# Kernel optimization log

Measured on AMD Instinct MI355X. Metric: run time of the kernel, lower is better.

The kernel has to match this reference:

```python
import jax, jax.numpy as jnp
import numpy as np

B, N, NODE_DIM, EDGE_DIM, H, L, Z, OUT = 4, 512, 16, 8, 64, 3, 64, 1
EPS = 1e-5  # torch BatchNorm1d default eps, training-mode batch stats


def _bn(x, g, b):
    # BatchNorm1d in training mode: biased batch mean/var over batch axis
    m = jnp.mean(x, axis=0)
    v = jnp.var(x, axis=0)
    return g * (x - m) * jax.lax.rsqrt(v + EPS) + b


def setup_inputs():
    keys = jax.random.split(jax.random.key(0), 16)

    def g(k, shape):
        fan = (shape[-2] + shape[-1]) if len(shape) >= 2 else 2 * shape[-1]
        return (jax.random.normal(k, shape) * np.sqrt(2.0 / fan)).astype(jnp.float32)

    return {
        'adj': (jax.random.uniform(keys[0], (B, N, N)) < 0.1).astype(jnp.float32),
        'node_feat': jax.random.normal(keys[1], (B, N, NODE_DIM), dtype=jnp.float32),
        'edge_feat': jax.random.normal(keys[2], (B, N, N, EDGE_DIM), dtype=jnp.float32),
        'nf1_w': g(keys[3], (NODE_DIM, 256)), 'nf1_b': jnp.zeros((256,), jnp.float32),
        'nf2_w': g(keys[4], (256, H)), 'nf2_b': jnp.zeros((H,), jnp.float32),
        'ef1_w': g(keys[5], (EDGE_DIM, 256)), 'ef1_b': jnp.zeros((256,), jnp.float32),
        'ef2_w': g(keys[6], (256, H)), 'ef2_b': jnp.zeros((H,), jnp.float32),
        'gcn_w': g(keys[7], (L, H, H)),
        'vn1_w': g(keys[8], (L, H, 2 * H)), 'vn1_b': jnp.zeros((L, 2 * H), jnp.float32),
        'vn1_g': jnp.ones((L, 2 * H), jnp.float32), 'vn1_be': jnp.zeros((L, 2 * H), jnp.float32),
        'vn2_w': g(keys[9], (L, 2 * H, H)), 'vn2_b': jnp.zeros((L, H), jnp.float32),
        'vn2_g': jnp.ones((L, H), jnp.float32), 'vn2_be': jnp.zeros((L, H), jnp.float32),
        'comb_w': g(keys[10], (L, 2 * H, H)), 'comb_b': jnp.zeros((L, H), jnp.float32),
        'lat1_w': g(keys[11], ((L + 1) * H, 256)), 'lat1_b': jnp.zeros((256,), jnp.float32),
        'lat2_w': g(keys[12], (256, Z)), 'lat2_b': jnp.zeros((Z,), jnp.float32),
        'fc1_w': g(keys[13], (Z, 512)), 'fc1_b': jnp.zeros((512,), jnp.float32),
        'fc2_w': g(keys[14], (512, OUT)), 'fc2_b': jnp.zeros((OUT,), jnp.float32),
    }


def _forward(adj, node_feat, edge_feat, nf1_w, nf1_b, nf2_w, nf2_b, ef1_w, ef1_b,
             ef2_w, ef2_b, gcn_w, vn1_w, vn1_b, vn1_g, vn1_be, vn2_w, vn2_b, vn2_g,
             vn2_be, comb_w, comb_b, lat1_w, lat1_b, lat2_w, lat2_b, fc1_w, fc1_b,
             fc2_w, fc2_b):
    # node / edge embedding MLPs
    nh = jnp.tanh(node_feat @ nf1_w + nf1_b)
    nh = jnp.tanh(nh @ nf2_w + nf2_b)                       # [B,N,H]
    eh = jnp.tanh(edge_feat @ ef1_w + ef1_b)
    eh = jnp.tanh(eh @ ef2_w + ef2_b)                       # [B,N,N,H]
    # einsum 'bijc,bjk->bik' sums over both j and c -> reduce c first
    e_sum = jnp.sum(eh, axis=-1)                            # [B,N,N]
    # GCN normalization: D = 1/rowsum(adj + I); identical every layer
    dinv = 1.0 / (jnp.sum(adj, axis=-1) + 1.0)
    adj_n = dinv[:, :, None] * adj                          # [B,N,N]
    hidden = nh
    alls = [nh]
    for l in range(L):
        hidden = jnp.tanh(adj_n @ (hidden @ gcn_w[l]))      # GraphConvSparse
        vn = jnp.mean(hidden, axis=1)                       # virtual-node pool [B,H]
        vn = jax.nn.relu(_bn(vn @ vn1_w[l] + vn1_b[l], vn1_g[l], vn1_be[l]))
        vn = jax.nn.relu(_bn(vn @ vn2_w[l] + vn2_b[l], vn2_g[l], vn2_be[l]))
        hidden = hidden + vn[:, None, :]                    # broadcast back to nodes
        gated = jnp.tanh(jnp.einsum('bij,bjk->bik', e_sum, hidden))
        hidden = jnp.tanh(jnp.concatenate([hidden, gated], axis=-1) @ comb_w[l] + comb_b[l])
        alls.append(hidden)
    lat = jnp.tanh(jnp.concatenate(alls, axis=-1) @ lat1_w + lat1_b)
    lat = jnp.tanh(lat @ lat2_w + lat2_b)                   # [B,N,Z]
    lat_sum = jnp.sum(lat, axis=1)                          # [B,Z]
    h = jnp.tanh(lat_sum @ fc1_w + fc1_b)
    predict = h @ fc2_w + fc2_b                             # [B,OUT]
    return predict, lat_sum


def reference(adj, node_feat, edge_feat, nf1_w, nf1_b, nf2_w, nf2_b, ef1_w, ef1_b,
              ef2_w, ef2_b, gcn_w, vn1_w, vn1_b, vn1_g, vn1_be, vn2_w, vn2_b, vn2_g,
              vn2_be, comb_w, comb_b, lat1_w, lat1_b, lat2_w, lat2_b, fc1_w, fc1_b,
              fc2_w, fc2_b):
    return _forward(adj, node_feat, edge_feat, nf1_w, nf1_b, nf2_w, nf2_b, ef1_w,
                    ef1_b, ef2_w, ef2_b, gcn_w, vn1_w, vn1_b, vn1_g, vn1_be, vn2_w,
                    vn2_b, vn2_g, vn2_be, comb_w, comb_b, lat1_w, lat1_b, lat2_w,
                    lat2_b, fc1_w, fc1_b, fc2_w, fc2_b)
```

## Files before the change

### kernel.cpp

```cpp
#include <hip/hip_runtime.h>
#include <math.h>

typedef unsigned short u16;
typedef unsigned int u32;

typedef __attribute__((ext_vector_type(8))) short short8;
typedef __attribute__((ext_vector_type(4))) float floatx4;

#define NTILES 16384

__device__ __forceinline__ float bfu(u16 u) { return __uint_as_float(((u32)u) << 16); }
__device__ __forceinline__ u16 f2bfs(float f) {
  u32 x = __float_as_uint(f);
  return (u16)((x + 0x7FFFu + ((x >> 16) & 1u)) >> 16);
}
__device__ __forceinline__ float tanh_fast(float x) {
  float e = __builtin_amdgcn_exp2f(x * 2.885390081777927f);
  return 1.0f - 2.0f * __builtin_amdgcn_rcpf(e + 1.0f);
}

__global__ __attribute__((amdgpu_flat_work_group_size(1024, 1024)))
__attribute__((amdgpu_waves_per_eu(4, 4)))
void k_edge(const float* __restrict__ ef,
    const float* __restrict__ w1, const float* __restrict__ b1,
    const float* __restrict__ w2, const float* __restrict__ b2,
    float* __restrict__ es32, u16* __restrict__ es16, int use16) {
  __shared__ __align__(16) short T1[16 * 2048];
  __shared__ __align__(16) short W2L[16384];
  __shared__ __align__(16) short W1L[2 * 2056];
  __shared__ __align__(16) float B1L[256];
  __shared__ __align__(16) float B2L[64];
  int t = threadIdx.x;
  int lane = t & 63, w = t >> 6, q = lane >> 4, r = lane & 15;

  for (int u = 0; u < 16; ++u) {
    int flat = u * 1024 + t;
    int k = flat >> 6, n = flat & 63;
    int c = k >> 3, j = k & 7;
    int physc = (c & 16) | ((c & 15) ^ (n & 15));
    W2L[(n * 32 + physc) * 8 + j] = (short)f2bfs(w2[flat]);
  }
  if (t < 512) {
    int hilo = t >> 8, idx = t & 255;
    int gu = idx >> 4, rr = idx & 15;
    int feat = (gu < 8) ? (rr * 8 + gu) : (120 + rr * 8 + gu);
    short8 v;
#pragma unroll
    for (int j = 0; j < 8; ++j) {
      float x = w1[j * 256 + feat];
      u32 xb = __float_as_uint(x);
      u16 hi = (u16)(xb >> 16);
      v[j] = hilo ? (short)f2bfs(x - bfu(hi)) : (short)hi;
    }
    *(short8*)&W1L[hilo * 2056 + idx * 8] = v;
  }
  if (t < 256) B1L[t] = b1[t];
  if (t < 64)  B2L[t] = b2[t];
  __syncthreads();

  short* t1w = &T1[w * 2048];
  const int hb = (q >> 1) * 2056;
  const int nw = gridDim.x * 16;
  int qt = blockIdx.x * 16 + w;
  float4 e0, e1;
  {
    const float4* ep = (const float4*)(ef + (size_t)qt * 128 + (size_t)r * 8);
    e0 = ep[0]; e1 = ep[1];
  }

  for (; qt < 4 * NTILES; qt += nw) {
    float ev[8] = {e0.x, e0.y, e0.z, e0.w, e1.x, e1.y, e1.z, e1.w};
    short8 af1;
#pragma unroll
    for (int j = 0; j < 8; ++j) {
      u32 xb = __float_as_uint(ev[j]);
      u16 hi = (u16)(xb >> 16);
      af1[j] = (q & 1) ? (short)f2bfs(ev[j] - bfu(hi)) : (short)hi;
    }
    int nqt = qt + nw;
    if (nqt < 4 * NTILES) {
      const float4* ep = (const float4*)(ef + (size_t)nqt * 128 + (size_t)r * 8);
      e0 = ep[0]; e1 = ep[1];
    }
    floatx4 acc4[4];
#pragma unroll
    for (int nt = 0; nt < 4; ++nt) acc4[nt] = (floatx4){0.f, 0.f, 0.f, 0.f};
#pragma unroll
    for (int ph = 0; ph < 2; ++ph) {
      floatx4 c1[8];
#pragma unroll
      for (int u = 0; u < 8; ++u) c1[u] = (floatx4){0.f, 0.f, 0.f, 0.f};
#pragma unroll
      for (int u = 0; u < 8; ++u) {
        short8 bf = *(const short8*)&W1L[hb + ((ph * 8 + u) * 16 + r) * 8];
        c1[u] = __builtin_amdgcn_mfma_f32_16x16x32_bf16(af1, bf, c1[u], 0, 0, 0);
      }
      asm volatile("s_waitcnt lgkmcnt(0)" ::: "memory");
      __builtin_amdgcn_sched_barrier(0);
      const float4* bp = (const float4*)&B1L[ph * 128 + r * 8];
      float4 bA = bp[0], bB = bp[1];
      float bias[8] = {bA.x, bA.y, bA.z, bA.w, bB.x, bB.y, bB.z, bB.w};
#pragma unroll
      for (int reg = 0; reg < 4; ++reg) {
        u32 pk[4];
#pragma unroll
        for (int p2 = 0; p2 < 4; ++p2) {
          float va = tanh_fast(c1[2 * p2][reg] + bias[2 * p2]);
          float vb = tanh_fast(c1[2 * p2 + 1][reg] + bias[2 * p2 + 1]);
          u32 pr;
          asm("v_cvt_pk_bf16_f32 %0, %1, %2" : "=v"(pr) : "v"(va), "v"(vb));
          pk[p2] = pr;
        }
        int row = q * 4 + reg;
        int physc = r ^ row;
        int4 wa; wa.x = (int)pk[0]; wa.y = (int)pk[1]; wa.z = (int)pk[2]; wa.w = (int)pk[3];
        *(int4*)&t1w[(row * 16 + physc) * 8] = wa;
      }
      asm volatile("s_waitcnt lgkmcnt(0)" ::: "memory");
      __builtin_amdgcn_sched_barrier(0);
#pragma unroll
      for (int sm = 0; sm < 4; ++sm) {
        int cc = (4 * sm + q) ^ r;
        short8 af = *(const short8*)&t1w[(r * 16 + cc) * 8];
        int wc = ph * 16 + cc;
#pragma unroll
        for (int nt = 0; nt < 4; ++nt) {
          short8 bf = *(const short8*)&W2L[((nt * 16 + r) * 32 + wc) * 8];
          acc4[nt] = __builtin_amdgcn_mfma_f32_16x16x32_bf16(af, bf, acc4[nt], 0, 0, 0);
        }
      }
    }
    float s0 = 0.f, s1 = 0.f, s2 = 0.f, s3 = 0.f;
#pragma unroll
    for (int nt = 0; nt < 4; ++nt) {
      float bb = B2L[nt * 16 + r];
      s0 += tanh_fast(acc4[nt][0] + bb);
      s1 += tanh_fast(acc4[nt][1] + bb);
      s2 += tanh_fast(acc4[nt][2] + bb);
      s3 += tanh_fast(acc4[nt][3] + bb);
    }
#pragma unroll
    for (int off = 1; off < 16; off <<= 1) {
      s0 += __shfl_xor(s0, off, 64);
      s1 += __shfl_xor(s1, off, 64);
      s2 += __shfl_xor(s2, off, 64);
      s3 += __shfl_xor(s3, off, 64);
    }
    if (r == 0) {
      int base = qt * 16 + q * 4;
      if (use16) {
        es16[base] = f2bfs(s0); es16[base + 1] = f2bfs(s1);
        es16[base + 2] = f2bfs(s2); es16[base + 3] = f2bfs(s3);
      } else {
        float4 o; o.x = s0; o.y = s1; o.z = s2; o.w = s3;
        *(float4*)&es32[base] = o;
      }
    }
  }
}

__global__ __launch_bounds__(256) void k_pre(const float* __restrict__ nf,
    const float* __restrict__ w1, const float* __restrict__ b1,
    const float* __restrict__ w2, const float* __restrict__ b2,
    const float* __restrict__ gw, const float* __restrict__ adj,
    float* __restrict__ hid, u16* __restrict__ alls16, float* __restrict__ tmp,
    float* __restrict__ dinv, int* __restrict__ cnt) {
  __shared__ float nfx[4][16];
  __shared__ float t1[4][256];
  __shared__ float nh[4][64];
  int t = threadIdx.x;
  int node0 = blockIdx.x * 4;
  if (blockIdx.x == 0 && t < 16) cnt[t] = 0;
  if (t < 64) nfx[t >> 4][t & 15] = nf[node0 * 16 + t];
  __syncthreads();
  float b1t = b1[t];
  float a0 = b1t, a1 = b1t, a2 = b1t, a3 = b1t;
#pragma unroll
  for (int c = 0; c < 16; ++c) {
    float wv = w1[c * 256 + t];
    a0 += nfx[0][c] * wv; a1 += nfx[1][c] * wv;
    a2 += nfx[2][c] * wv; a3 += nfx[3][c] * wv;
  }
  t1[0][t] = tanh_fast(a0); t1[1][t] = tanh_fast(a1);
  t1[2][t] = tanh_fast(a2); t1[3][t] = tanh_fast(a3);
  __syncthreads();
  int nl = t >> 6, h = t & 63;
  {
    float acc = b2[h];
    for (int c = 0; c < 256; c += 4) {
      float4 xv = *(const float4*)&t1[nl][c];
      acc += xv.x * w2[c * 64 + h] + xv.y * w2[(c + 1) * 64 + h]
           + xv.z * w2[(c + 2) * 64 + h] + xv.w * w2[(c + 3) * 64 + h];
    }
    float v = tanh_fast(acc);
    int node = node0 + nl;
    hid[node * 64 + h] = v;
    alls16[node * 256 + h] = f2bfs(v);
    nh[nl][h] = v;
  }
  __syncthreads();
  {
    float g = 0.f;
    for (int c = 0; c < 64; ++c) g += nh[nl][c] * gw[c * 64 + h];
    tmp[(node0 + nl) * 64 + h] = g;
  }
  {
    int lane = t & 63, row = node0 + (t >> 6);
    float s = 0.f;
#pragma unroll
    for (int u = 0; u < 8; ++u) s += adj[(size_t)row * 512 + u * 64 + lane];
#pragma unroll
    for (int off = 32; off > 0; off >>= 1) s += __shfl_xor(s, off, 64);
    if (lane == 0) dinv[row] = 1.0f / (s + 1.0f);
  }
}

__global__ __launch_bounds__(256) void k_adjmm0(const float* __restrict__ adj,
    const float* __restrict__ X, const float* __restrict__ dinv,
    float* __restrict__ out, float* __restrict__ vnpart, int* cnt,
    const float* __restrict__ vw1, const float* __restrict__ vb1,
    const float* __restrict__ vg1, const float* __restrict__ vbe1,
    const float* __restrict__ vw2, const float* __restrict__ vb2,
    const float* __restrict__ vg2, const float* __restrict__ vbe2,
    float* __restrict__ vnout, int l) {
  __shared__ float Xt[64 * 64];
  __shared__ float Al[8 * 65];
  __shared__ floatx4 red4[256];
  __shared__ int isLast;
  int t = threadIdx.x;
  int b = blockIdx.x >> 6, it = blockIdx.x & 63;
  int hq = t & 15, slot = t >> 4, row = slot & 7, half = slot >> 3;
  floatx4 acc = (floatx4){0.f, 0.f, 0.f, 0.f};
  for (int jt = 0; jt < 8; ++jt) {
    __syncthreads();
    for (int u = 0; u < 16; ++u) {
      int idx = u * 256 + t;
      int jl = idx >> 6, hh = idx & 63;
      Xt[idx] = X[(b * 512 + jt * 64 + jl) * 64 + hh];
    }
#pragma unroll
    for (int u = 0; u < 2; ++u) {
      int idx = u * 256 + t;
      int il = idx >> 6, jl = idx & 63;
      Al[il * 65 + jl] = adj[((size_t)(b * 512 + it * 8 + il)) * 512 + jt * 64 + jl];
    }
    __syncthreads();
    const float* xp = &Xt[(half * 32) * 64 + hq * 4];
    const float* ap = &Al[row * 65 + half * 32];
#pragma unroll
    for (int jl = 0; jl < 32; ++jl) {
      floatx4 xv = *(const floatx4*)(xp + jl * 64);
      float a = ap[jl];
      acc[0] += a * xv[0]; acc[1] += a * xv[1];
      acc[2] += a * xv[2]; acc[3] += a * xv[3];
    }
  }
  red4[t] = acc;
  __syncthreads();
  if (t < 128) {
    floatx4 s = red4[t], s2 = red4[t + 128];
    int gr = b * 512 + it * 8 + row;
    float d = dinv[gr];
    floatx4 o;
#pragma unroll
    for (int i = 0; i < 4; ++i) o[i] = tanh_fast((s[i] + s2[i]) * d);
    *(floatx4*)&out[gr * 64 + hq * 4] = o;
    red4[t] = o;
  }
  __syncthreads();
  if (t < 16) {
    floatx4 ssum = (floatx4){0.f, 0.f, 0.f, 0.f};
#pragma unroll
    for (int r2 = 0; r2 < 8; ++r2) {
      floatx4 v = red4[r2 * 16 + t];
      ssum[0] += v[0]; ssum[1] += v[1]; ssum[2] += v[2]; ssum[3] += v[3];
    }
    *(floatx4*)&vnpart[(b * 64 + it) * 64 + t * 4] = ssum;
  }
  __threadfence();
  __syncthreads();
  if (t == 0) isLast = (atomicAdd(cnt, 1) == 255);
  __syncthreads();
  if (isLast) {
    __threadfence();
    float* x0 = Xt; float* x1 = Xt + 256; float* y1 = Xt + 768; float* x2 = Xt + 1280;
    {
      int bb = t >> 6, h = t & 63;
      float s = 0.f;
      for (int c = 0; c < 64; ++c) s += vnpart[(bb * 64 + c) * 64 + h];
      x0[t] = s * (1.0f / 512.0f);
    }
    __syncthreads();
    for (int rep = 0; rep < 2; ++rep) {
      int idx = rep * 256 + t;
      int bb = idx >> 7, j = idx & 127;
      float a = vb1[l * 128 + j];
      for (int h = 0; h < 64; ++h) a += x0[bb * 64 + h] * vw1[l * 8192 + h * 128 + j];
      x1[idx] = a;
    }
    __syncthreads();
    if (t < 128) {
      int j = t;
      float a = x1[j], bq = x1[128 + j], c = x1[256 + j], d = x1[384 + j];
      float m = 0.25f * (a + bq + c + d);
      float da = a - m, db = bq - m, dc = c - m, dd = d - m;
      float var = 0.25f * (da * da + db * db + dc * dc + dd * dd);
      float sc = vg1[l * 128 + j] / sqrtf(var + 1e-5f);
      float be = vbe1[l * 128 + j];
      y1[j]       = fmaxf(sc * da + be, 0.f);
      y1[128 + j] = fmaxf(sc * db + be, 0.f);
      y1[256 + j] = fmaxf(sc * dc + be, 0.f);
      y1[384 + j] = fmaxf(sc * dd + be, 0.f);
    }
    __syncthreads();
    {
      int bb = t >> 6, k = t & 63;
      float a = vb2[l * 64 + k];
      for (int j = 0; j < 128; ++j) a += y1[bb * 128 + j] * vw2[l * 8192 + j * 64 + k];
      x2[t] = a;
    }
    __syncthreads();
    if (t < 64) {
      int k = t;
      float a = x2[k], bq = x2[64 + k], c = x2[128 + k], d = x2[192 + k];
      float m = 0.25f * (a + bq + c + d);
      float da = a - m, db = bq - m, dc = c - m, dd = d - m;
      float var = 0.25f * (da * da + db * db + dc * dc + dd * dd);
      float sc = vg2[l * 64 + k] / sqrtf(var + 1e-5f);
      float be = vbe2[l * 64 + k];
      vnout[k]       = fmaxf(sc * da + be, 0.f);
      vnout[64 + k]  = fmaxf(sc * db + be, 0.f);
      vnout[128 + k] = fmaxf(sc * dc + be, 0.f);
      vnout[192 + k] = fmaxf(sc * dd + be, 0.f);
    }
  }
}

__global__ __launch_bounds__(256) void k_gate_comb(
    const float* __restrict__ es32, const u16* __restrict__ es16, int use16,
    const float* __restrict__ hid, const float* __restrict__ vnin,
    const float* __restrict__ cw, const float* __restrict__ cb,
    const float* __restrict__ gw_next,
    u16* __restrict__ alls16, float* __restrict__ tmpout, int l, int do_gcn) {
  __shared__ float Xt[64 * 64];
  __shared__ float Al[8 * 65];
  __shared__ floatx4 red4[256];
  __shared__ float gatedL[8 * 64];
  __shared__ float catL[8 * 128];
  __shared__ float hnL[8 * 64];
  int t = threadIdx.x;
  int b = blockIdx.x >> 6, it = blockIdx.x & 63;
  int hq = t & 15, slot = t >> 4, row = slot & 7, half = slot >> 3;
  floatx4 acc = (floatx4){0.f, 0.f, 0.f, 0.f};
  for (int jt = 0; jt < 8; ++jt) {
    __syncthreads();
    for (int u = 0; u < 16; ++u) {
      int idx = u * 256 + t;
      int jl = idx >> 6, hh = idx & 63;
      Xt[idx] = hid[(b * 512 + jt * 64 + jl) * 64 + hh] + vnin[b * 64 + hh];
    }
#pragma unroll
    for (int u = 0; u < 2; ++u) {
      int idx = u * 256 + t;
      int il = idx >> 6, jl = idx & 63;
      size_t ai = ((size_t)(b * 512 + it * 8 + il)) * 512 + jt * 64 + jl;
      Al[il * 65 + jl] = use16 ? bfu(es16[ai]) : es32[ai];
    }
    __syncthreads();
    const float* xp = &Xt[(half * 32) * 64 + hq * 4];
    const float* ap = &Al[row * 65 + half * 32];
#pragma unroll
    for (int jl = 0; jl < 32; ++jl) {
      floatx4 xv = *(const floatx4*)(xp + jl * 64);
      float a = ap[jl];
      acc[0] += a * xv[0]; acc[1] += a * xv[1];
      acc[2] += a * xv[2]; acc[3] += a * xv[3];
    }
  }
  red4[t] = acc;
  __syncthreads();
  if (t < 128) {
    floatx4 s = red4[t], s2 = red4[t + 128];
    floatx4 o;
#pragma unroll
    for (int i = 0; i < 4; ++i) o[i] = tanh_fast(s[i] + s2[i]);
    *(floatx4*)&gatedL[row * 64 + hq * 4] = o;
  }
  __syncthreads();
#pragma unroll
  for (int u = 0; u < 4; ++u) {
    int idx = u * 256 + t;
    int nl = idx >> 7, c = idx & 127;
    int node = b * 512 + it * 8 + nl;
    catL[idx] = (c < 64) ? (hid[node * 64 + c] + vnin[b * 64 + c])
                         : gatedL[nl * 64 + (c - 64)];
  }
  __syncthreads();
  int nl = t >> 6, h = t & 63;
  float a0 = cb[l * 64 + h], a1 = a0;
  const float* wp = cw + l * 8192 + h;
  for (int c = 0; c < 128; ++c) {
    float wv = wp[c * 64];
    a0 += catL[nl * 128 + c] * wv;
    a1 += catL[(nl + 4) * 128 + c] * wv;
  }
  float v0 = tanh_fast(a0), v1 = tanh_fast(a1);
  int n0 = b * 512 + it * 8 + nl, n1 = n0 + 4;
  alls16[n0 * 256 + (l + 1) * 64 + h] = f2bfs(v0);
  alls16[n1 * 256 + (l + 1) * 64 + h] = f2bfs(v1);
  if (do_gcn) {
    hnL[nl * 64 + h] = v0;
    hnL[(nl + 4) * 64 + h] = v1;
    __syncthreads();
    float g0 = 0.f, g1 = 0.f;
    for (int c = 0; c < 64; ++c) {
      float wv = gw_next[c * 64 + h];
      g0 += hnL[nl * 64 + c] * wv;
      g1 += hnL[(nl + 4) * 64 + c] * wv;
    }
    tmpout[n0 * 64 + h] = g0;
    tmpout[n1 * 64 + h] = g1;
  }
}

__global__ __launch_bounds__(512) void k_lat(const u16* __restrict__ alls16,
    const float* __restrict__ w1, const float* __restrict__ bb1,
    const float* __restrict__ w2, const float* __restrict__ bb2,
    float* __restrict__ latpart) {
  __shared__ float x[8][256];
  __shared__ float t1[8][256];
  __shared__ float red[8][256];
  int t = threadIdx.x;
  int g = t >> 8, tt = t & 255;
  int b = blockIdx.x >> 6, chunk = blockIdx.x & 63;
#pragma unroll
  for (int u = 0; u < 4; ++u)
    x[g * 4 + u][tt] = bfu(alls16[(size_t)(b * 512 + chunk * 8 + g * 4 + u) * 256 + tt]);
  __syncthreads();
  float a1[4];
  float bb = bb1[tt];
#pragma unroll
  for (int u = 0; u < 4; ++u) a1[u] = bb;
  for (int c = 0; c < 256; ++c) {
    float wv = w1[c * 256 + tt];
#pragma unroll
    for (int u = 0; u < 4; ++u) a1[u] += x[g * 4 + u][c] * wv;
  }
#pragma unroll
  for (int u = 0; u < 4; ++u) t1[g * 4 + u][tt] = tanh_fast(a1[u]);
  __syncthreads();
  int quar = tt >> 6, k = tt & 63, c0 = quar * 64;
  float a2[4];
#pragma unroll
  for (int u = 0; u < 4; ++u) a2[u] = 0.f;
  for (int c = 0; c < 64; ++c) {
    float wv = w2[(c0 + c) * 64 + k];
#pragma unroll
    for (int u = 0; u < 4; ++u) a2[u] += t1[g * 4 + u][c0 + c] * wv;
  }
#pragma unroll
  for (int u = 0; u < 4; ++u) red[g * 4 + u][tt] = a2[u];
  __syncthreads();
  if (t < 64) {
    float acc2 = 0.f;
    float b2v = bb2[t];
#pragma unroll
    for (int u = 0; u < 8; ++u) {
      float s = red[u][t] + red[u][t + 64] + red[u][t + 128] + red[u][t + 192] + b2v;
      acc2 += tanh_fast(s);
    }
    latpart[(b * 64 + chunk) * 64 + t] = acc2;
  }
}

__global__ __launch_bounds__(512) void k_final(const float* __restrict__ latpart,
    const float* __restrict__ f1w, const float* __restrict__ f1b,
    const float* __restrict__ f2w, const float* __restrict__ f2b,
    float* __restrict__ outp) {
  __shared__ float lred[512];
  __shared__ float ls[64];
  __shared__ float wred[8];
  int b = blockIdx.x, t = threadIdx.x;
  int z = t & 63, cg = t >> 6;
  float s = 0.f;
  for (int c = cg * 8; c < cg * 8 + 8; ++c) s += latpart[(b * 64 + c) * 64 + z];
  lred[t] = s;
  __syncthreads();
  if (t < 64) {
    float ssum = 0.f;
    for (int gg = 0; gg < 8; ++gg) ssum += lred[gg * 64 + t];
    ls[t] = ssum;
    outp[4 + b * 64 + t] = ssum;
  }
  __syncthreads();
  float acc = f1b[t];
  for (int zz = 0; zz < 64; ++zz) acc += ls[zz] * f1w[zz * 512 + t];
  float h = tanh_fast(acc);
  float p = h * f2w[t];
#pragma unroll
  for (int off = 32; off > 0; off >>= 1) p += __shfl_xor(p, off, 64);
  if ((t & 63) == 0) wred[t >> 6] = p;
  __syncthreads();
  if (t == 0) {
    float a = 0.f;
    for (int wv = 0; wv < 8; ++wv) a += wred[wv];
    outp[b] = a + f2b[0];
  }
}

extern "C" void kernel_launch(void* const* d_in, const int* in_sizes, int n_in,
                              void* d_out, int out_size, void* d_ws, size_t ws_size,
                              hipStream_t stream) {
  const float* adj       = (const float*)d_in[0];
  const float* node_feat = (const float*)d_in[1];
  const float* edge_feat = (const float*)d_in[2];
  const float* nf1_w = (const float*)d_in[3];
  const float* nf1_b = (const float*)d_in[4];
  const float* nf2_w = (const float*)d_in[5];
  const float* nf2_b = (const float*)d_in[6];
  const float* ef1_w = (const float*)d_in[7];
  const float* ef1_b = (const float*)d_in[8];
  const float* ef2_w = (const float*)d_in[9];
  const float* ef2_b = (const float*)d_in[10];
  const float* gcn_w = (const float*)d_in[11];
  const float* vn1_w = (const float*)d_in[12];
  const float* vn1_b = (const float*)d_in[13];
  const float* vn1_g = (const float*)d_in[14];
  const float* vn1_be = (const float*)d_in[15];
  const float* vn2_w = (const float*)d_in[16];
  const float* vn2_b = (const float*)d_in[17];
  const float* vn2_g = (const float*)d_in[18];
  const float* vn2_be = (const float*)d_in[19];
  const float* comb_w = (const float*)d_in[20];
  const float* comb_b = (const float*)d_in[21];
  const float* lat1_w = (const float*)d_in[22];
  const float* lat1_b = (const float*)d_in[23];
  const float* lat2_w = (const float*)d_in[24];
  const float* lat2_b = (const float*)d_in[25];
  const float* fc1_w = (const float*)d_in[26];
  const float* fc1_b = (const float*)d_in[27];
  const float* fc2_w = (const float*)d_in[28];
  const float* fc2_b = (const float*)d_in[29];

  const int use16 = (ws_size < (size_t)12 * 1024 * 1024) ? 1 : 0;
  char* p = (char*)d_ws;
  float* es32 = (float*)p;
  u16*   es16 = (u16*)p;
  size_t es_bytes = use16 ? (size_t)1048576 * 2 : (size_t)1048576 * 4;
  u16*   alls16  = (u16*)(p + es_bytes);
  float* hid     = (float*)(alls16 + 524288);
  float* tmp     = hid + 131072;
  float* dinv    = tmp + 131072;
  float* vnpart  = dinv + 2048;
  float* vn      = vnpart + 16384;
  float* latpart = vn + 256;
  int*   cnt     = (int*)(latpart + 16384);

  k_pre<<<512, 256, 0, stream>>>(node_feat, nf1_w, nf1_b, nf2_w, nf2_b,
                                 gcn_w, adj, hid, alls16, tmp, dinv, cnt);
  k_edge<<<256, 1024, 0, stream>>>(edge_feat, ef1_w, ef1_b, ef2_w, ef2_b,
                                   es32, es16, use16);
  for (int l = 0; l < 3; ++l) {
    k_adjmm0<<<256, 256, 0, stream>>>(adj, tmp, dinv, hid, vnpart, cnt + l,
        vn1_w, vn1_b, vn1_g, vn1_be, vn2_w, vn2_b, vn2_g, vn2_be, vn, l);
    k_gate_comb<<<256, 256, 0, stream>>>(es32, es16, use16, hid, vn,
        comb_w, comb_b, gcn_w + (l + 1) * 4096, alls16, tmp, l, (l < 2) ? 1 : 0);
  }
  k_lat<<<256, 512, 0, stream>>>(alls16, lat1_w, lat1_b, lat2_w, lat2_b, latpart);
  k_final<<<4, 512, 0, stream>>>(latpart, fc1_w, fc1_b, fc2_w, fc2_b,
                                 (float*)d_out);
}
```

Before: 435.6 us.

## Halve rows per block and register-prefetch next tiles in adjacency matmul kernels

k_adjmm0 and k_gate_comb now give each block 4 node rows instead of 8, which doubles the grid to 512 blocks, and the inter-block counter and vnpart layout are resized to match. Each thread loads the next 64-column X and adjacency tile into registers while the current tile is computed from shared memory, so global-load latency overlaps the FMA loop. The aim is more blocks to fill the CUs and fewer stalls on global memory. In exchange, each X tile is re-read by twice as many blocks, more registers are used, and the per-block split of the reduction shrinks.

```diff
diff --git a/kernel.cpp b/kernel.cpp
--- a/kernel.cpp
+++ b/kernel.cpp
@@ -224,31 +224,40 @@
     const float* __restrict__ vg2, const float* __restrict__ vbe2,
     float* __restrict__ vnout, int l) {
   __shared__ float Xt[64 * 64];
-  __shared__ float Al[8 * 65];
+  __shared__ float Al[4 * 65];
   __shared__ floatx4 red4[256];
+  __shared__ floatx4 vnp4[64];
   __shared__ int isLast;
   int t = threadIdx.x;
-  int b = blockIdx.x >> 6, it = blockIdx.x & 63;
-  int hq = t & 15, slot = t >> 4, row = slot & 7, half = slot >> 3;
+  int b = blockIdx.x >> 7, blk = blockIdx.x & 127;
+  int hq = t & 15, slot = t >> 4, row = slot & 3, half = slot >> 2;
   floatx4 acc = (floatx4){0.f, 0.f, 0.f, 0.f};
+  float xreg[16], areg;
+  int il = t >> 6, jl2 = t & 63;
+#pragma unroll
+  for (int u = 0; u < 16; ++u) {
+    int jl = (u * 256 + t) >> 6;
+    xreg[u] = X[(b * 512 + jl) * 64 + jl2];
+  }
+  areg = adj[((size_t)(b * 512 + blk * 4 + il)) * 512 + jl2];
   for (int jt = 0; jt < 8; ++jt) {
     __syncthreads();
-    for (int u = 0; u < 16; ++u) {
-      int idx = u * 256 + t;
-      int jl = idx >> 6, hh = idx & 63;
-      Xt[idx] = X[(b * 512 + jt * 64 + jl) * 64 + hh];
-    }
-#pragma unroll
-    for (int u = 0; u < 2; ++u) {
-      int idx = u * 256 + t;
-      int il = idx >> 6, jl = idx & 63;
-      Al[il * 65 + jl] = adj[((size_t)(b * 512 + it * 8 + il)) * 512 + jt * 64 + jl];
-    }
-    __syncthreads();
-    const float* xp = &Xt[(half * 32) * 64 + hq * 4];
-    const float* ap = &Al[row * 65 + half * 32];
-#pragma unroll
-    for (int jl = 0; jl < 32; ++jl) {
+#pragma unroll
+    for (int u = 0; u < 16; ++u) Xt[u * 256 + t] = xreg[u];
+    Al[il * 65 + jl2] = areg;
+    __syncthreads();
+    if (jt < 7) {
+#pragma unroll
+      for (int u = 0; u < 16; ++u) {
+        int jl = (u * 256 + t) >> 6;
+        xreg[u] = X[(b * 512 + (jt + 1) * 64 + jl) * 64 + jl2];
+      }
+      areg = adj[((size_t)(b * 512 + blk * 4 + il)) * 512 + (jt + 1) * 64 + jl2];
+    }
+    const float* xp = &Xt[(half * 16) * 64 + hq * 4];
+    const float* ap = &Al[row * 65 + half * 16];
+#pragma unroll
+    for (int jl = 0; jl < 16; ++jl) {
       floatx4 xv = *(const floatx4*)(xp + jl * 64);
       float a = ap[jl];
       acc[0] += a * xv[0]; acc[1] += a * xv[1];
@@ -257,29 +266,27 @@
   }
   red4[t] = acc;
   __syncthreads();
-  if (t < 128) {
-    floatx4 s = red4[t], s2 = red4[t + 128];
-    int gr = b * 512 + it * 8 + row;
+  if (t < 64) {
+    floatx4 s0 = red4[t], s1 = red4[t + 64], s2 = red4[t + 128], s3 = red4[t + 192];
+    int gr = b * 512 + blk * 4 + (t >> 4);
     float d = dinv[gr];
     floatx4 o;
 #pragma unroll
-    for (int i = 0; i < 4; ++i) o[i] = tanh_fast((s[i] + s2[i]) * d);
-    *(floatx4*)&out[gr * 64 + hq * 4] = o;
-    red4[t] = o;
+    for (int i = 0; i < 4; ++i) o[i] = tanh_fast((((s0[i] + s1[i]) + s2[i]) + s3[i]) * d);
+    *(floatx4*)&out[gr * 64 + (t & 15) * 4] = o;
+    vnp4[t] = o;
   }
   __syncthreads();
   if (t < 16) {
-    floatx4 ssum = (floatx4){0.f, 0.f, 0.f, 0.f};
-#pragma unroll
-    for (int r2 = 0; r2 < 8; ++r2) {
-      floatx4 v = red4[r2 * 16 + t];
-      ssum[0] += v[0]; ssum[1] += v[1]; ssum[2] += v[2]; ssum[3] += v[3];
-    }
-    *(floatx4*)&vnpart[(b * 64 + it) * 64 + t * 4] = ssum;
+    floatx4 s = vnp4[t], s1 = vnp4[16 + t], s2 = vnp4[32 + t], s3 = vnp4[48 + t];
+    floatx4 ss;
+#pragma unroll
+    for (int i = 0; i < 4; ++i) ss[i] = ((s[i] + s1[i]) + s2[i]) + s3[i];
+    *(floatx4*)&vnpart[(b * 128 + blk) * 64 + t * 4] = ss;
   }
   __threadfence();
   __syncthreads();
-  if (t == 0) isLast = (atomicAdd(cnt, 1) == 255);
+  if (t == 0) isLast = (atomicAdd(cnt, 1) == 511);
   __syncthreads();
   if (isLast) {
     __threadfence();
@@ -287,7 +294,7 @@
     {
       int bb = t >> 6, h = t & 63;
       float s = 0.f;
-      for (int c = 0; c < 64; ++c) s += vnpart[(bb * 64 + c) * 64 + h];
+      for (int c = 0; c < 128; ++c) s += vnpart[(bb * 128 + c) * 64 + h];
       x0[t] = s * (1.0f / 512.0f);
     }
     __syncthreads();
@@ -343,34 +350,46 @@
     const float* __restrict__ gw_next,
     u16* __restrict__ alls16, float* __restrict__ tmpout, int l, int do_gcn) {
   __shared__ float Xt[64 * 64];
-  __shared__ float Al[8 * 65];
+  __shared__ float Al[4 * 65];
   __shared__ floatx4 red4[256];
-  __shared__ float gatedL[8 * 64];
-  __shared__ float catL[8 * 128];
-  __shared__ float hnL[8 * 64];
+  __shared__ float gatedL[4 * 64];
+  __shared__ float catL[4 * 128];
+  __shared__ float hnL[4 * 64];
   int t = threadIdx.x;
-  int b = blockIdx.x >> 6, it = blockIdx.x & 63;
-  int hq = t & 15, slot = t >> 4, row = slot & 7, half = slot >> 3;
+  int b = blockIdx.x >> 7, blk = blockIdx.x & 127;
+  int hq = t & 15, slot = t >> 4, row = slot & 3, half = slot >> 2;
+  int il = t >> 6, jl2 = t & 63;
+  float vnl = vnin[b * 64 + jl2];
   floatx4 acc = (floatx4){0.f, 0.f, 0.f, 0.f};
+  float xreg[16], areg;
+#pragma unroll
+  for (int u = 0; u < 16; ++u) {
+    int jl = (u * 256 + t) >> 6;
+    xreg[u] = hid[(b * 512 + jl) * 64 + jl2];
+  }
+  {
+    size_t ai = ((size_t)(b * 512 + blk * 4 + il)) * 512 + jl2;
+    areg = use16 ? bfu(es16[ai]) : es32[ai];
+  }
   for (int jt = 0; jt < 8; ++jt) {
     __syncthreads();
-    for (int u = 0; u < 16; ++u) {
-      int idx = u * 256 + t;
-      int jl = idx >> 6, hh = idx & 63;
-      Xt[idx] = hid[(b * 512 + jt * 64 + jl) * 64 + hh] + vnin[b * 64 + hh];
-    }
-#pragma unroll
-    for (int u = 0; u < 2; ++u) {
-      int idx = u * 256 + t;
-      int il = idx >> 6, jl = idx & 63;
-      size_t ai = ((size_t)(b * 512 + it * 8 + il)) * 512 + jt * 64 + jl;
-      Al[il * 65 + jl] = use16 ? bfu(es16[ai]) : es32[ai];
-    }
-    __syncthreads();
-    const float* xp = &Xt[(half * 32) * 64 + hq * 4];
-    const float* ap = &Al[row * 65 + half * 32];
-#pragma unroll
-    for (int jl = 0; jl < 32; ++jl) {
+#pragma unroll
+    for (int u = 0; u < 16; ++u) Xt[u * 256 + t] = xreg[u] + vnl;
+    Al[il * 65 + jl2] = areg;
+    __syncthreads();
+    if (jt < 7) {
+#pragma unroll
+      for (int u = 0; u < 16; ++u) {
+        int jl = (u * 256 + t) >> 6;
+        xreg[u] = hid[(b * 512 + (jt + 1) * 64 + jl) * 64 + jl2];
+      }
+      size_t ai = ((size_t)(b * 512 + blk * 4 + il)) * 512 + (jt + 1) * 64 + jl2;
+      areg = use16 ? bfu(es16[ai]) : es32[ai];
+    }
+    const float* xp = &Xt[(half * 16) * 64 + hq * 4];
+    const float* ap = &Al[row * 65 + half * 16];
+#pragma unroll
+    for (int jl = 0; jl < 16; ++jl) {
       floatx4 xv = *(const floatx4*)(xp + jl * 64);
       float a = ap[jl];
       acc[0] += a * xv[0]; acc[1] += a * xv[1];
@@ -379,47 +398,36 @@
   }
   red4[t] = acc;
   __syncthreads();
-  if (t < 128) {
-    floatx4 s = red4[t], s2 = red4[t + 128];
+  if (t < 64) {
+    floatx4 s0 = red4[t], s1 = red4[t + 64], s2 = red4[t + 128], s3 = red4[t + 192];
     floatx4 o;
 #pragma unroll
-    for (int i = 0; i < 4; ++i) o[i] = tanh_fast(s[i] + s2[i]);
-    *(floatx4*)&gatedL[row * 64 + hq * 4] = o;
-  }
-  __syncthreads();
-#pragma unroll
-  for (int u = 0; u < 4; ++u) {
+    for (int i = 0; i < 4; ++i) o[i] = tanh_fast(((s0[i] + s1[i]) + s2[i]) + s3[i]);
+    *(floatx4*)&gatedL[(t >> 4) * 64 + (t & 15) * 4] = o;
+  }
+  __syncthreads();
+#pragma unroll
+  for (int u = 0; u < 2; ++u) {
     int idx = u * 256 + t;
     int nl = idx >> 7, c = idx & 127;
-    int node = b * 512 + it * 8 + nl;
+    int node = b * 512 + blk * 4 + nl;
     catL[idx] = (c < 64) ? (hid[node * 64 + c] + vnin[b * 64 + c])
                          : gatedL[nl * 64 + (c - 64)];
   }
   __syncthreads();
   int nl = t >> 6, h = t & 63;
-  float a0 = cb[l * 64 + h], a1 = a0;
+  float a = cb[l * 64 + h];
   const float* wp = cw + l * 8192 + h;
-  for (int c = 0; c < 128; ++c) {
-    float wv = wp[c * 64];
-    a0 += catL[nl * 128 + c] * wv;
-    a1 += catL[(nl + 4) * 128 + c] * wv;
-  }
-  float v0 = tanh_fast(a0), v1 = tanh_fast(a1);
-  int n0 = b * 512 + it * 8 + nl, n1 = n0 + 4;
-  alls16[n0 * 256 + (l + 1) * 64 + h] = f2bfs(v0);
-  alls16[n1 * 256 + (l + 1) * 64 + h] = f2bfs(v1);
+  for (int c = 0; c < 128; ++c) a += catL[nl * 128 + c] * wp[c * 64];
+  float v = tanh_fast(a);
+  int node = b * 512 + blk * 4 + nl;
+  alls16[(size_t)node * 256 + (l + 1) * 64 + h] = f2bfs(v);
   if (do_gcn) {
-    hnL[nl * 64 + h] = v0;
-    hnL[(nl + 4) * 64 + h] = v1;
-    __syncthreads();
-    float g0 = 0.f, g1 = 0.f;
-    for (int c = 0; c < 64; ++c) {
-      float wv = gw_next[c * 64 + h];
-      g0 += hnL[nl * 64 + c] * wv;
-      g1 += hnL[(nl + 4) * 64 + c] * wv;
-    }
-    tmpout[n0 * 64 + h] = g0;
-    tmpout[n1 * 64 + h] = g1;
+    hnL[nl * 64 + h] = v;
+    __syncthreads();
+    float g = 0.f;
+    for (int c = 0; c < 64; ++c) g += hnL[nl * 64 + c] * gw_next[c * 64 + h];
+    tmpout[node * 64 + h] = g;
   }
 }
 
@@ -552,7 +560,7 @@
   float* tmp     = hid + 131072;
   float* dinv    = tmp + 131072;
   float* vnpart  = dinv + 2048;
-  float* vn      = vnpart + 16384;
+  float* vn      = vnpart + 32768;
   float* latpart = vn + 256;
   int*   cnt     = (int*)(latpart + 16384);
 
@@ -561,9 +569,9 @@
   k_edge<<<256, 1024, 0, stream>>>(edge_feat, ef1_w, ef1_b, ef2_w, ef2_b,
                                    es32, es16, use16);
   for (int l = 0; l < 3; ++l) {
-    k_adjmm0<<<256, 256, 0, stream>>>(adj, tmp, dinv, hid, vnpart, cnt + l,
+    k_adjmm0<<<512, 256, 0, stream>>>(adj, tmp, dinv, hid, vnpart, cnt + l,
         vn1_w, vn1_b, vn1_g, vn1_be, vn2_w, vn2_b, vn2_g, vn2_be, vn, l);
-    k_gate_comb<<<256, 256, 0, stream>>>(es32, es16, use16, hid, vn,
+    k_gate_comb<<<512, 256, 0, stream>>>(es32, es16, use16, hid, vn,
         comb_w, comb_b, gcn_w + (l + 1) * 4096, alls16, tmp, l, (l < 2) ? 1 : 0);
   }
   k_lat<<<256, 512, 0, stream>>>(alls16, lat1_w, lat1_b, lat2_w, lat2_b, latpart);
```

New measurement: 481.3 us. 10.5% more time.
